# Kernel optimization log

Hardware: AMD Instinct MI355X
Metric: run time of the kernel (lower is better)

The kernel has to match this reference:

```python
import jax, jax.numpy as jnp
import numpy as np
import math

B, T, D = 2, 2048, 1024
H = 16
HD = D // H
DFF = 4096
EPS = 1e-5


def setup_inputs() -> dict:
    key = jax.random.key(0)
    ks = jax.random.split(key, 11)
    s = 0.02
    return {
        "x": jax.random.normal(ks[0], (B, T, D), dtype=jnp.float32),
        "scale1": jnp.ones((D,), jnp.float32),
        "scale2": jnp.ones((D,), jnp.float32),
        "Wqkv": jax.random.normal(ks[1], (D, 3 * D), jnp.float32) * s,
        "bqkv": jnp.zeros((3 * D,), jnp.float32),
        "Wo": jax.random.normal(ks[2], (D, D), jnp.float32) * s,
        "bo": jnp.zeros((D,), jnp.float32),
        "W1": jax.random.normal(ks[3], (D, DFF), jnp.float32) * s,
        "b1": jnp.zeros((DFF,), jnp.float32),
        "W2": jax.random.normal(ks[4], (DFF, D), jnp.float32) * s,
        "b2": jnp.zeros((D,), jnp.float32),
    }


def rmsnorm(x, scale):
    # Faithful to source: norm = ||x||/sqrt(d); out = scale * x / (norm + eps)
    d = x.shape[-1]
    norm = jnp.linalg.norm(x, axis=-1, keepdims=True) * (1.0 / math.sqrt(d))
    return scale * x / (norm + EPS)


def attention(x, Wqkv, bqkv, Wo, bo):
    b, t, c = x.shape
    qkv = x @ Wqkv + bqkv                       # [B,T,3D]
    qkv = qkv.reshape(b, t, 3, H, HD)
    q, k, v = qkv[:, :, 0], qkv[:, :, 1], qkv[:, :, 2]   # [B,T,H,HD]
    scores = jnp.einsum("bqhd,bkhd->bhqk", q, k) / math.sqrt(HD)
    w = jax.nn.softmax(scores, axis=-1)
    out = jnp.einsum("bhqk,bkhd->bqhd", w, v).reshape(b, t, c)
    return out @ Wo + bo


def reference(x, scale1, scale2, Wqkv, bqkv, Wo, bo, W1, b1, W2, b2):
    x = x + attention(rmsnorm(x, scale1), Wqkv, bqkv, Wo, bo)
    h = rmsnorm(x, scale2)
    ff = (jax.nn.gelu(h @ W1 + b1, approximate=False)) @ W2 + b2
    return x + ff
```

## Files before the change

### kernel.cpp

```cpp
#include <hip/hip_runtime.h>
#include <hip/hip_bf16.h>
#include <math.h>

typedef unsigned short u16;
typedef __bf16 bf16x8 __attribute__((ext_vector_type(8)));
typedef float f32x4 __attribute__((ext_vector_type(4)));
typedef unsigned int u32x2 __attribute__((ext_vector_type(2)));

#define B_   2
#define T_   2048
#define D_   1024
#define H_   16
#define HD_  64
#define DFF_ 4096
#define M_TOK (B_*T_)

__device__ __forceinline__ u16 f2bf(float f){
  unsigned u = __float_as_uint(f);
  u += 0x7fff + ((u>>16)&1);
  return (u16)(u>>16);
}

__device__ __forceinline__ void gl2lds16(const void* g, void* l){
  __builtin_amdgcn_global_load_lds((const __attribute__((address_space(1))) void*)g,
                                   (__attribute__((address_space(3))) void*)l, 16, 0, 0);
}

__device__ __forceinline__ unsigned lds_u32(const void* p){
  return (unsigned)(uintptr_t)(const __attribute__((address_space(3))) void*)p;
}

__device__ __forceinline__ u32x2 tr_read(unsigned addr){
  u32x2 d;
  asm volatile("ds_read_b64_tr_b16 %0, %1" : "=v"(d) : "v"(addr));
  return d;
}
__device__ __forceinline__ u32x2 tr_read512(unsigned addr){
  u32x2 d;
  asm volatile("ds_read_b64_tr_b16 %0, %1 offset:512" : "=v"(d) : "v"(addr));
  return d;
}
__device__ __forceinline__ bf16x8 pack8(u32x2 a, u32x2 b){
  union { u32x2 u[2]; bf16x8 v; } x; x.u[0]=a; x.u[1]=b; return x.v;
}
__device__ __forceinline__ unsigned cvt_pk_bf16(float a, float b){
  unsigned r;
  asm("v_cvt_pk_bf16_f32 %0, %1, %2" : "=v"(r) : "v"(a), "v"(b));
  return r;
}

__global__ __launch_bounds__(256) void k_transpose_bf16(const float* __restrict__ in,
                                                        u16* __restrict__ out, int K, int N){
  __shared__ float t[32][33];
  int bx = blockIdx.x*32, by = blockIdx.y*32;
  int tx = threadIdx.x, ty = threadIdx.y;
  #pragma unroll
  for(int i=ty;i<32;i+=8) t[i][tx] = in[(size_t)(by+i)*N + bx + tx];
  __syncthreads();
  #pragma unroll
  for(int i=ty;i<32;i+=8) out[(size_t)(bx+i)*K + by + tx] = f2bf(t[tx][i]);
}

__global__ __launch_bounds__(256) void k_rmsnorm_bf16(const float* __restrict__ x,
                                                      const float* __restrict__ scale,
                                                      u16* __restrict__ out){
  int row = blockIdx.x;
  int tid = threadIdx.x;
  int lane = tid&63, wave = tid>>6;
  const float4* xr = (const float4*)(x + (size_t)row*D_);
  float4 v = xr[tid];
  float ss = v.x*v.x + v.y*v.y + v.z*v.z + v.w*v.w;
  #pragma unroll
  for(int o=1;o<64;o<<=1) ss += __shfl_xor(ss, o);
  __shared__ float red[4];
  if(lane==0) red[wave]=ss;
  __syncthreads();
  float tot = red[0]+red[1]+red[2]+red[3];
  float inv = 1.0f/(sqrtf(tot*(1.0f/D_)) + 1e-5f);
  const float4* sr = (const float4*)scale;
  float4 s4 = sr[tid];
  u16* o4 = out + (size_t)row*D_ + tid*4;
  o4[0]=f2bf(v.x*s4.x*inv); o4[1]=f2bf(v.y*s4.y*inv);
  o4[2]=f2bf(v.z*s4.z*inv); o4[3]=f2bf(v.w*s4.w*inv);
}

template<int EPI>
__global__ __launch_bounds__(256) void k_gemm(const u16* __restrict__ A, const u16* __restrict__ Bt,
                                              const float* __restrict__ bias, const float* __restrict__ res,
                                              void* __restrict__ Cout, int M, int N, int K){
  __shared__ u16 As[128*32];
  __shared__ u16 Bs[128*32];
  int tid = threadIdx.x;
  int lane = tid&63, wave = tid>>6;
  int wr = wave>>1, wc = wave&1;
  int row0 = blockIdx.x*128, col0 = blockIdx.y*128;
  f32x4 acc[4][4];
  #pragma unroll
  for(int m=0;m<4;m++)
    #pragma unroll
    for(int n=0;n<4;n++) acc[m][n] = (f32x4){0.f,0.f,0.f,0.f};
  const u16* Ag = A + (size_t)row0*K;
  const u16* Bg = Bt + (size_t)col0*K;
  for(int k0=0;k0<K;k0+=32){
    __syncthreads();
    #pragma unroll
    for(int c=tid;c<512;c+=256){
      gl2lds16(Ag + (size_t)(c>>2)*K + k0 + (c&3)*8, (char*)As + c*16);
      gl2lds16(Bg + (size_t)(c>>2)*K + k0 + (c&3)*8, (char*)Bs + c*16);
    }
    __syncthreads();
    const u16* ab = As + (wr*64 + (lane&15))*32 + (lane>>4)*8;
    const u16* bb = Bs + (wc*64 + (lane&15))*32 + (lane>>4)*8;
    bf16x8 a[4], b[4];
    #pragma unroll
    for(int m=0;m<4;m++) a[m] = *(const bf16x8*)(ab + m*16*32);
    #pragma unroll
    for(int n=0;n<4;n++) b[n] = *(const bf16x8*)(bb + n*16*32);
    #pragma unroll
    for(int m=0;m<4;m++)
      #pragma unroll
      for(int n=0;n<4;n++)
        acc[m][n] = __builtin_amdgcn_mfma_f32_16x16x32_bf16(a[m], b[n], acc[m][n], 0,0,0);
  }
  #pragma unroll
  for(int m=0;m<4;m++){
    #pragma unroll
    for(int n=0;n<4;n++){
      #pragma unroll
      for(int r=0;r<4;r++){
        int row = row0 + wr*64 + m*16 + (lane>>4)*4 + r;
        int col = col0 + wc*64 + n*16 + (lane&15);
        float v = acc[m][n][r] + bias[col];
        if constexpr(EPI==1){
          ((float*)Cout)[(size_t)row*N + col] = v + res[(size_t)row*N + col];
        } else if constexpr(EPI==2){
          v = 0.5f*v*(1.0f + erff(v*0.70710678118f));
          ((u16*)Cout)[(size_t)row*N + col] = f2bf(v);
        } else {
          ((u16*)Cout)[(size_t)row*N + col] = f2bf(v);
        }
      }
    }
  }
}

__global__ __launch_bounds__(256) void k_gemm_pk(const u16* __restrict__ A, const u16* __restrict__ Bt,
                                                 float* __restrict__ P, int M, int N, int K){
  __shared__ u16 As[128*32];
  __shared__ u16 Bs[128*32];
  int tid = threadIdx.x;
  int lane = tid&63, wave = tid>>6;
  int wr = wave>>1, wc = wave&1;
  int row0 = blockIdx.x*128, col0 = blockIdx.y*128;
  int kc = blockIdx.z;
  int klen = K/2, kbeg = kc*klen;
  f32x4 acc[4][4];
  #pragma unroll
  for(int m=0;m<4;m++)
    #pragma unroll
    for(int n=0;n<4;n++) acc[m][n] = (f32x4){0.f,0.f,0.f,0.f};
  const u16* Ag = A + (size_t)row0*K + kbeg;
  const u16* Bg = Bt + (size_t)col0*K + kbeg;
  for(int k0=0;k0<klen;k0+=32){
    __syncthreads();
    #pragma unroll
    for(int c=tid;c<512;c+=256){
      gl2lds16(Ag + (size_t)(c>>2)*K + k0 + (c&3)*8, (char*)As + c*16);
      gl2lds16(Bg + (size_t)(c>>2)*K + k0 + (c&3)*8, (char*)Bs + c*16);
    }
    __syncthreads();
    const u16* ab = As + (wr*64 + (lane&15))*32 + (lane>>4)*8;
    const u16* bb = Bs + (wc*64 + (lane&15))*32 + (lane>>4)*8;
    bf16x8 a[4], b[4];
    #pragma unroll
    for(int m=0;m<4;m++) a[m] = *(const bf16x8*)(ab + m*16*32);
    #pragma unroll
    for(int n=0;n<4;n++) b[n] = *(const bf16x8*)(bb + n*16*32);
    #pragma unroll
    for(int m=0;m<4;m++)
      #pragma unroll
      for(int n=0;n<4;n++)
        acc[m][n] = __builtin_amdgcn_mfma_f32_16x16x32_bf16(a[m], b[n], acc[m][n], 0,0,0);
  }
  float* Pk = P + (size_t)kc*M*N;
  #pragma unroll
  for(int m=0;m<4;m++)
    #pragma unroll
    for(int n=0;n<4;n++)
      #pragma unroll
      for(int r=0;r<4;r++){
        int row = row0 + wr*64 + m*16 + (lane>>4)*4 + r;
        int col = col0 + wc*64 + n*16 + (lane&15);
        Pk[(size_t)row*N + col] = acc[m][n][r];
      }
}

__global__ __launch_bounds__(256) void k_ff2_reduce(const float* __restrict__ P,
                                                    const float* __restrict__ bias,
                                                    const float* __restrict__ res,
                                                    float* __restrict__ out){
  const size_t total4 = (size_t)M_TOK*D_/4;
  const float4* p0 = (const float4*)P;
  const float4* p1 = (const float4*)(P + (size_t)M_TOK*D_);
  const float4* rr = (const float4*)res;
  const float4* bb = (const float4*)bias;
  float4* oo = (float4*)out;
  for(size_t i = (size_t)blockIdx.x*256 + threadIdx.x; i < total4; i += (size_t)gridDim.x*256){
    float4 a = p0[i], b = p1[i], r = rr[i], c = bb[i & (D_/4 - 1)];
    float4 o;
    o.x = (a.x+b.x)+(c.x+r.x);
    o.y = (a.y+b.y)+(c.y+r.y);
    o.z = (a.z+b.z)+(c.z+r.z);
    o.w = (a.w+b.w)+(c.w+r.w);
    oo[i] = o;
  }
}

__global__ __launch_bounds__(256,4) void k_attn(const u16* __restrict__ qkv, u16* __restrict__ O){
  __shared__ alignas(16) u16 Ks[2][4096];
  __shared__ alignas(16) u16 Vs[2][4096];
  __shared__ alignas(16) u16 Ps[4][1024];
  const int qt = blockIdx.x, h = blockIdx.y, b = blockIdx.z;
  const int tid = threadIdx.x, lane = tid&63, wave = tid>>6;
  const int lo = lane&15, hi = lane>>4, l7 = lane&7;
  const u16* qkvB = qkv + (size_t)b*T_*3072;
  const int hoff = h*64;
  const float C2 = 0.18033688f;

  const int q0 = qt*64 + wave*16;
  const u16* qp = qkvB + (size_t)(q0+lo)*3072 + hoff + hi*8;
  bf16x8 aq0 = *(const bf16x8*)qp;
  bf16x8 aq1 = *(const bf16x8*)(qp+32);

  size_t sK[2], sV[2];
  {
    int cc[2] = {tid, tid+256};
    #pragma unroll
    for(int i=0;i<2;i++){
      int c = cc[i];
      sK[i] = (size_t)(c>>3)*3072 + 1024 + hoff + (((c&7)^((c>>3)&7))<<3);
      int kv = ((c>>5)<<2) + ((c>>1)&3);
      int d0 = (((c&31)>>3)<<4) | ((c&1)<<3);
      sV[i] = (size_t)kv*3072 + 2048 + hoff + d0;
    }
  }
  const unsigned kb0 = (unsigned)lo*128 + (unsigned)((hi^l7))*16;
  const unsigned kb1 = (unsigned)lo*128 + (unsigned)(((hi|4)^l7))*16;
  const unsigned vtr = (unsigned)hi*1024 + (unsigned)lo*2;
  const unsigned swzQ = (unsigned)(lo&7)<<4;

  f32x4 oac[4];
  #pragma unroll
  for(int n=0;n<4;n++) oac[n] = (f32x4){0.f,0.f,0.f,0.f};
  float mrow = -1e30f;
  float lsum = 0.f;

  {
    char* kd = (char*)Ks[0]; char* vd = (char*)Vs[0];
    gl2lds16(qkvB + sK[0], kd + tid*16);
    gl2lds16(qkvB + sK[1], kd + tid*16 + 4096);
    gl2lds16(qkvB + sV[0], vd + tid*16);
    gl2lds16(qkvB + sV[1], vd + tid*16 + 4096);
  }
  int buf = 0;
  for(int t=0;t<T_/64;t++){
    __syncthreads();
    if(t < T_/64-1){
      size_t koff = (size_t)(t+1)*64*3072;
      char* kd = (char*)Ks[buf^1]; char* vd = (char*)Vs[buf^1];
      gl2lds16(qkvB + koff + sK[0], kd + tid*16);
      gl2lds16(qkvB + koff + sK[1], kd + tid*16 + 4096);
      gl2lds16(qkvB + koff + sV[0], vd + tid*16);
      gl2lds16(qkvB + koff + sV[1], vd + tid*16 + 4096);
    }
    const char* K_ = (const char*)Ks[buf];
    u16* P_ = Ps[wave];

    f32x4 s[4];
    __builtin_amdgcn_s_setprio(1);
    #pragma unroll
    for(int n=0;n<4;n++){
      bf16x8 k0f = *(const bf16x8*)(K_ + n*2048 + kb0);
      bf16x8 k1f = *(const bf16x8*)(K_ + n*2048 + kb1);
      f32x4 z = (f32x4){0.f,0.f,0.f,0.f};
      z = __builtin_amdgcn_mfma_f32_16x16x32_bf16(k0f, aq0, z, 0,0,0);
      z = __builtin_amdgcn_mfma_f32_16x16x32_bf16(k1f, aq1, z, 0,0,0);
      s[n] = z;
    }
    __builtin_amdgcn_s_setprio(0);

    float mx = s[0][0];
    #pragma unroll
    for(int n=0;n<4;n++)
      #pragma unroll
      for(int r=0;r<4;r++) mx = fmaxf(mx, s[n][r]);

    if(!__all(mx <= mrow + 64.0f)){
      float mm = fmaxf(mx, __shfl_xor(mx,16));
      mm = fmaxf(mm, __shfl_xor(mm,32));
      float nm = fmaxf(mrow, mm);
      float alpha = exp2f((mrow - nm)*C2);
      mrow = nm;
      lsum *= alpha;
      float ar[4];
      #pragma unroll
      for(int r=0;r<4;r++) ar[r] = __shfl(alpha, hi*4 + r);
      #pragma unroll
      for(int n=0;n<4;n++)
        #pragma unroll
        for(int r=0;r<4;r++) oac[n][r] *= ar[r];
    }

    const float nmC2 = -mrow*C2;
    #pragma unroll
    for(int n=0;n<4;n++){
      float p0v = exp2f(fmaf(s[n][0], C2, nmC2));
      float p1v = exp2f(fmaf(s[n][1], C2, nmC2));
      float p2v = exp2f(fmaf(s[n][2], C2, nmC2));
      float p3v = exp2f(fmaf(s[n][3], C2, nmC2));
      lsum += (p0v+p1v)+(p2v+p3v);
      u32x2 pw;
      pw[0] = cvt_pk_bf16(p0v, p1v);
      pw[1] = cvt_pk_bf16(p2v, p3v);
      *(u32x2*)((char*)P_ + (unsigned)lo*128 + (((unsigned)(n*32 + hi*8)) ^ swzQ)) = pw;
    }

    const unsigned vsb = lds_u32(Vs[buf]);
    #pragma unroll
    for(int kk=0;kk<2;kk++){
      bf16x8 ap = *(const bf16x8*)((const char*)P_ + (kk==0 ? kb0 : kb1));
      u32x2 t0[4], t1[4];
      #pragma unroll
      for(int n=0;n<4;n++){
        unsigned a = vsb + vtr + (unsigned)kk*4096 + (unsigned)n*128;
        t0[n] = tr_read(a);
        t1[n] = tr_read512(a);
      }
      asm volatile("s_waitcnt lgkmcnt(0)" ::: "memory");
      __builtin_amdgcn_sched_barrier(0);
      __builtin_amdgcn_s_setprio(1);
      #pragma unroll
      for(int n=0;n<4;n++){
        bf16x8 bv = pack8(t0[n], t1[n]);
        oac[n] = __builtin_amdgcn_mfma_f32_16x16x32_bf16(ap, bv, oac[n], 0,0,0);
      }
      __builtin_amdgcn_s_setprio(0);
    }
    buf ^= 1;
  }

  lsum += __shfl_xor(lsum, 16);
  lsum += __shfl_xor(lsum, 32);
  float linv = 1.0f/lsum;
  float lr[4];
  #pragma unroll
  for(int r=0;r<4;r++) lr[r] = __shfl(linv, hi*4 + r);
  size_t obase = ((size_t)b*T_ + q0)*D_ + hoff;
  #pragma unroll
  for(int n=0;n<4;n++)
    #pragma unroll
    for(int r=0;r<4;r++)
      O[obase + (size_t)(hi*4+r)*D_ + n*16 + lo] = f2bf(oac[n][r]*lr[r]);
}

extern "C" void kernel_launch(void* const* d_in, const int* in_sizes, int n_in,
                              void* d_out, int out_size, void* d_ws, size_t ws_size,
                              hipStream_t stream){
  (void)in_sizes; (void)n_in; (void)out_size; (void)ws_size;
  const float* x      = (const float*)d_in[0];
  const float* scale1 = (const float*)d_in[1];
  const float* scale2 = (const float*)d_in[2];
  const float* Wqkv   = (const float*)d_in[3];
  const float* bqkv   = (const float*)d_in[4];
  const float* Wo     = (const float*)d_in[5];
  const float* bo     = (const float*)d_in[6];
  const float* W1     = (const float*)d_in[7];
  const float* b1     = (const float*)d_in[8];
  const float* W2     = (const float*)d_in[9];
  const float* b2     = (const float*)d_in[10];
  float* out = (float*)d_out;

  char* w = (char*)d_ws;
  u16* xn1   = (u16*)w;  w += (size_t)M_TOK*D_*2;
  u16* qkvb  = (u16*)w;  w += (size_t)M_TOK*3*D_*2;
  u16* Obuf  = (u16*)w;  w += (size_t)M_TOK*D_*2;
  float* x2  = (float*)w; w += (size_t)M_TOK*D_*4;
  u16* xn2   = (u16*)w;  w += (size_t)M_TOK*D_*2;
  u16* h1    = (u16*)w;  w += (size_t)M_TOK*DFF_*2;
  u16* Wqkvt = (u16*)w;  w += (size_t)3*D_*D_*2;
  u16* Wot   = (u16*)w;  w += (size_t)D_*D_*2;
  u16* W1t   = (u16*)w;  w += (size_t)D_*DFF_*2;
  u16* W2t   = (u16*)w;  w += (size_t)DFF_*D_*2;
  float* pk  = (float*)d_ws;

  dim3 tb(32,8);
  k_transpose_bf16<<<dim3(3*D_/32, D_/32), tb, 0, stream>>>(Wqkv, Wqkvt, D_, 3*D_);
  k_transpose_bf16<<<dim3(D_/32,   D_/32), tb, 0, stream>>>(Wo,   Wot,   D_, D_);
  k_transpose_bf16<<<dim3(DFF_/32, D_/32), tb, 0, stream>>>(W1,   W1t,   D_, DFF_);
  k_transpose_bf16<<<dim3(D_/32, DFF_/32), tb, 0, stream>>>(W2,   W2t,   DFF_, D_);

  k_rmsnorm_bf16<<<M_TOK, 256, 0, stream>>>(x, scale1, xn1);
  k_gemm<0><<<dim3(M_TOK/128, 3*D_/128), 256, 0, stream>>>(xn1, Wqkvt, bqkv, nullptr, qkvb, M_TOK, 3*D_, D_);
  k_attn<<<dim3(T_/64, H_, B_), 256, 0, stream>>>(qkvb, Obuf);
  k_gemm<1><<<dim3(M_TOK/128, D_/128), 256, 0, stream>>>(Obuf, Wot, bo, x, x2, M_TOK, D_, D_);
  k_rmsnorm_bf16<<<M_TOK, 256, 0, stream>>>(x2, scale2, xn2);
  k_gemm<2><<<dim3(M_TOK/128, DFF_/128), 256, 0, stream>>>(xn2, W1t, b1, nullptr, h1, M_TOK, DFF_, D_);
  k_gemm_pk<<<dim3(M_TOK/128, D_/128, 2), 256, 0, stream>>>(h1, W2t, pk, M_TOK, D_, DFF_);
  k_ff2_reduce<<<2048, 256, 0, stream>>>(pk, b2, x2, out);
}
```

Measured before the change: 284.1 us.

## Add 256x256 multi-stage pipelined GEMM and XOR-swizzle LDS layouts

Measured after the change: 272.7 us. 1.04x faster.

```diff
diff --git a/kernel.cpp b/kernel.cpp
--- a/kernel.cpp
+++ b/kernel.cpp
@@ -47,6 +47,13 @@
   unsigned r;
   asm("v_cvt_pk_bf16_f32 %0, %1, %2" : "=v"(r) : "v"(a), "v"(b));
   return r;
+}
+
+__device__ __forceinline__ void block_barrier(){
+  asm volatile("" ::: "memory");
+  __builtin_amdgcn_s_barrier();
+  __builtin_amdgcn_sched_barrier(0);
+  asm volatile("" ::: "memory");
 }
 
 __global__ __launch_bounds__(256) void k_transpose_bf16(const float* __restrict__ in,
@@ -85,6 +92,95 @@
 }
 
 template<int EPI>
+__global__ __launch_bounds__(512,2) void k_gemm256(const u16* __restrict__ A, const u16* __restrict__ Bt,
+                                                   const float* __restrict__ bias,
+                                                   void* __restrict__ Cout, int M, int N, int K){
+  __shared__ u16 LDS[4][16384];
+  const int tid = threadIdx.x;
+  const int lane = tid&63, wave = tid>>6;
+  const int lo = lane&15, hi = lane>>4;
+  const int wm = wave>>2, wn = wave&3;
+  const int row0 = blockIdx.x*256, col0 = blockIdx.y*256;
+  f32x4 acc[8][4];
+  #pragma unroll
+  for(int m=0;m<8;m++)
+    #pragma unroll
+    for(int n=0;n<4;n++) acc[m][n] = (f32x4){0.f,0.f,0.f,0.f};
+  const u16* Ag = A + (size_t)row0*K;
+  const u16* Bg = Bt + (size_t)col0*K;
+  const int NT = K>>5;
+
+  const int cc0 = tid, cc1 = tid+512;
+  const size_t s0 = (size_t)(cc0>>2)*K + (size_t)((((cc0&3)^((cc0>>3)&3)))<<3);
+  const size_t s1 = (size_t)(cc1>>2)*K + (size_t)((((cc1&3)^((cc1>>3)&3)))<<3);
+
+  #define STAGE_A(t) { const u16* Ab = Ag + (size_t)(t)*32; char* d = (char*)LDS[(t)&3]; \
+    gl2lds16(Ab + s0, d + cc0*16); gl2lds16(Ab + s1, d + cc1*16); }
+  #define STAGE_B(t) { const u16* Bb = Bg + (size_t)(t)*32; char* d = (char*)LDS[(t)&3] + 16384; \
+    gl2lds16(Bb + s0, d + cc0*16); gl2lds16(Bb + s1, d + cc1*16); }
+
+  STAGE_A(0); STAGE_B(0); STAGE_A(1); STAGE_B(1); STAGE_A(2); STAGE_B(2);
+
+  const unsigned slot = (unsigned)((hi ^ ((lo>>1)&3))<<4);
+  for(int t=0;t<NT;t++){
+    if(t<NT-2)       { asm volatile("s_waitcnt vmcnt(8)" ::: "memory"); }
+    else if(t==NT-2) { asm volatile("s_waitcnt vmcnt(4)" ::: "memory"); }
+    else             { asm volatile("s_waitcnt vmcnt(0)" ::: "memory"); }
+    block_barrier();
+    const char* bufp = (const char*)LDS[t&3];
+    const char* ap = bufp + (wm*128 + lo)*64 + slot;
+    const char* bp = bufp + 16384 + (wn*64 + lo)*64 + slot;
+
+    if(t+3<NT) STAGE_A(t+3);
+    __builtin_amdgcn_sched_barrier(0);
+    bf16x8 a0[4], b[4];
+    #pragma unroll
+    for(int m=0;m<4;m++) a0[m] = *(const bf16x8*)(ap + m*1024);
+    #pragma unroll
+    for(int n=0;n<4;n++) b[n]  = *(const bf16x8*)(bp + n*1024);
+    __builtin_amdgcn_s_setprio(1);
+    #pragma unroll
+    for(int m=0;m<4;m++)
+      #pragma unroll
+      for(int n=0;n<4;n++)
+        acc[m][n] = __builtin_amdgcn_mfma_f32_16x16x32_bf16(a0[m], b[n], acc[m][n], 0,0,0);
+    __builtin_amdgcn_s_setprio(0);
+
+    if(t+3<NT) STAGE_B(t+3);
+    __builtin_amdgcn_sched_barrier(0);
+    bf16x8 a1[4];
+    #pragma unroll
+    for(int m=0;m<4;m++) a1[m] = *(const bf16x8*)(ap + 4096 + m*1024);
+    __builtin_amdgcn_s_setprio(1);
+    #pragma unroll
+    for(int m=0;m<4;m++)
+      #pragma unroll
+      for(int n=0;n<4;n++)
+        acc[m+4][n] = __builtin_amdgcn_mfma_f32_16x16x32_bf16(a1[m], b[n], acc[m+4][n], 0,0,0);
+    __builtin_amdgcn_s_setprio(0);
+  }
+  #undef STAGE_A
+  #undef STAGE_B
+
+  #pragma unroll
+  for(int m=0;m<8;m++){
+    #pragma unroll
+    for(int n=0;n<4;n++){
+      #pragma unroll
+      for(int r=0;r<4;r++){
+        int row = row0 + wm*128 + m*16 + hi*4 + r;
+        int col = col0 + wn*64 + n*16 + lo;
+        float v = acc[m][n][r] + bias[col];
+        if constexpr(EPI==2){
+          v = 0.5f*v*(1.0f + erff(v*0.70710678118f));
+        }
+        ((u16*)Cout)[(size_t)row*N + col] = f2bf(v);
+      }
+    }
+  }
+}
+
+template<int EPI>
 __global__ __launch_bounds__(256) void k_gemm(const u16* __restrict__ A, const u16* __restrict__ Bt,
                                               const float* __restrict__ bias, const float* __restrict__ res,
                                               void* __restrict__ Cout, int M, int N, int K){
@@ -92,6 +188,7 @@
   __shared__ u16 Bs[128*32];
   int tid = threadIdx.x;
   int lane = tid&63, wave = tid>>6;
+  int lo = lane&15, hi = lane>>4;
   int wr = wave>>1, wc = wave&1;
   int row0 = blockIdx.x*128, col0 = blockIdx.y*128;
   f32x4 acc[4][4];
@@ -101,21 +198,22 @@
     for(int n=0;n<4;n++) acc[m][n] = (f32x4){0.f,0.f,0.f,0.f};
   const u16* Ag = A + (size_t)row0*K;
   const u16* Bg = Bt + (size_t)col0*K;
+  const unsigned sw = (unsigned)((hi^((lo>>1)&3))*16);
   for(int k0=0;k0<K;k0+=32){
     __syncthreads();
     #pragma unroll
     for(int c=tid;c<512;c+=256){
-      gl2lds16(Ag + (size_t)(c>>2)*K + k0 + (c&3)*8, (char*)As + c*16);
-      gl2lds16(Bg + (size_t)(c>>2)*K + k0 + (c&3)*8, (char*)Bs + c*16);
+      gl2lds16(Ag + (size_t)(c>>2)*K + k0 + (size_t)(((c&3)^((c>>3)&3))<<3), (char*)As + c*16);
+      gl2lds16(Bg + (size_t)(c>>2)*K + k0 + (size_t)(((c&3)^((c>>3)&3))<<3), (char*)Bs + c*16);
     }
     __syncthreads();
-    const u16* ab = As + (wr*64 + (lane&15))*32 + (lane>>4)*8;
-    const u16* bb = Bs + (wc*64 + (lane&15))*32 + (lane>>4)*8;
+    const char* ab = (const char*)As + (wr*64+lo)*64;
+    const char* bb = (const char*)Bs + (wc*64+lo)*64;
     bf16x8 a[4], b[4];
     #pragma unroll
-    for(int m=0;m<4;m++) a[m] = *(const bf16x8*)(ab + m*16*32);
-    #pragma unroll
-    for(int n=0;n<4;n++) b[n] = *(const bf16x8*)(bb + n*16*32);
+    for(int m=0;m<4;m++) a[m] = *(const bf16x8*)(ab + m*1024 + sw);
+    #pragma unroll
+    for(int n=0;n<4;n++) b[n] = *(const bf16x8*)(bb + n*1024 + sw);
     #pragma unroll
     for(int m=0;m<4;m++)
       #pragma unroll
@@ -128,8 +226,8 @@
     for(int n=0;n<4;n++){
       #pragma unroll
       for(int r=0;r<4;r++){
-        int row = row0 + wr*64 + m*16 + (lane>>4)*4 + r;
-        int col = col0 + wc*64 + n*16 + (lane&15);
+        int row = row0 + wr*64 + m*16 + hi*4 + r;
+        int col = col0 + wc*64 + n*16 + lo;
         float v = acc[m][n][r] + bias[col];
         if constexpr(EPI==1){
           ((float*)Cout)[(size_t)row*N + col] = v + res[(size_t)row*N + col];
@@ -150,6 +248,7 @@
   __shared__ u16 Bs[128*32];
   int tid = threadIdx.x;
   int lane = tid&63, wave = tid>>6;
+  int lo = lane&15, hi = lane>>4;
   int wr = wave>>1, wc = wave&1;
   int row0 = blockIdx.x*128, col0 = blockIdx.y*128;
   int kc = blockIdx.z;
@@ -161,21 +260,22 @@
     for(int n=0;n<4;n++) acc[m][n] = (f32x4){0.f,0.f,0.f,0.f};
   const u16* Ag = A + (size_t)row0*K + kbeg;
   const u16* Bg = Bt + (size_t)col0*K + kbeg;
+  const unsigned sw = (unsigned)((hi^((lo>>1)&3))*16);
   for(int k0=0;k0<klen;k0+=32){
     __syncthreads();
     #pragma unroll
     for(int c=tid;c<512;c+=256){
-      gl2lds16(Ag + (size_t)(c>>2)*K + k0 + (c&3)*8, (char*)As + c*16);
-      gl2lds16(Bg + (size_t)(c>>2)*K + k0 + (c&3)*8, (char*)Bs + c*16);
+      gl2lds16(Ag + (size_t)(c>>2)*K + k0 + (size_t)(((c&3)^((c>>3)&3))<<3), (char*)As + c*16);
+      gl2lds16(Bg + (size_t)(c>>2)*K + k0 + (size_t)(((c&3)^((c>>3)&3))<<3), (char*)Bs + c*16);
     }
     __syncthreads();
-    const u16* ab = As + (wr*64 + (lane&15))*32 + (lane>>4)*8;
-    const u16* bb = Bs + (wc*64 + (lane&15))*32 + (lane>>4)*8;
+    const char* ab = (const char*)As + (wr*64+lo)*64;
+    const char* bb = (const char*)Bs + (wc*64+lo)*64;
     bf16x8 a[4], b[4];
     #pragma unroll
-    for(int m=0;m<4;m++) a[m] = *(const bf16x8*)(ab + m*16*32);
-    #pragma unroll
-    for(int n=0;n<4;n++) b[n] = *(const bf16x8*)(bb + n*16*32);
+    for(int m=0;m<4;m++) a[m] = *(const bf16x8*)(ab + m*1024 + sw);
+    #pragma unroll
+    for(int n=0;n<4;n++) b[n] = *(const bf16x8*)(bb + n*1024 + sw);
     #pragma unroll
     for(int m=0;m<4;m++)
       #pragma unroll
@@ -189,8 +289,8 @@
     for(int n=0;n<4;n++)
       #pragma unroll
       for(int r=0;r<4;r++){
-        int row = row0 + wr*64 + m*16 + (lane>>4)*4 + r;
-        int col = col0 + wc*64 + n*16 + (lane&15);
+        int row = row0 + wr*64 + m*16 + hi*4 + r;
+        int col = col0 + wc*64 + n*16 + lo;
         Pk[(size_t)row*N + col] = acc[m][n][r];
       }
 }
@@ -400,11 +500,11 @@
   k_transpose_bf16<<<dim3(D_/32, DFF_/32), tb, 0, stream>>>(W2,   W2t,   DFF_, D_);
 
   k_rmsnorm_bf16<<<M_TOK, 256, 0, stream>>>(x, scale1, xn1);
-  k_gemm<0><<<dim3(M_TOK/128, 3*D_/128), 256, 0, stream>>>(xn1, Wqkvt, bqkv, nullptr, qkvb, M_TOK, 3*D_, D_);
+  k_gemm256<0><<<dim3(M_TOK/256, 3*D_/256), 512, 0, stream>>>(xn1, Wqkvt, bqkv, qkvb, M_TOK, 3*D_, D_);
   k_attn<<<dim3(T_/64, H_, B_), 256, 0, stream>>>(qkvb, Obuf);
   k_gemm<1><<<dim3(M_TOK/128, D_/128), 256, 0, stream>>>(Obuf, Wot, bo, x, x2, M_TOK, D_, D_);
   k_rmsnorm_bf16<<<M_TOK, 256, 0, stream>>>(x2, scale2, xn2);
-  k_gemm<2><<<dim3(M_TOK/128, DFF_/128), 256, 0, stream>>>(xn2, W1t, b1, nullptr, h1, M_TOK, DFF_, D_);
+  k_gemm256<2><<<dim3(M_TOK/256, DFF_/256), 512, 0, stream>>>(xn2, W1t, b1, h1, M_TOK, DFF_, D_);
   k_gemm_pk<<<dim3(M_TOK/128, D_/128, 2), 256, 0, stream>>>(h1, W2t, pk, M_TOK, D_, DFF_);
   k_ff2_reduce<<<2048, 256, 0, stream>>>(pk, b2, x2, out);
 }
```
